# Performance work log

Hardware: AMD Instinct MI355X
Metric: run time of the kernel (lower is better)

The kernel has to match this reference:

```python
import jax, jax.numpy as jnp
import numpy as np

USER_NUM = 100000
ITEM_NUM = 50000
E = 128   # embedding_size
A = 64    # attention_size
M = 8     # memory_size
B = 4096  # batch
NF = 50   # friends per user


def _l2norm(x, axis):
    # torch F.normalize(p=2): x / max(||x||, eps)
    n = jnp.sqrt(jnp.sum(x * x, axis=axis, keepdims=True))
    return x / jnp.maximum(n, 1e-12)


def setup_inputs() -> dict:
    key = jax.random.key(0)
    ks = jax.random.split(key, 9)
    u = lambda k, shape: jax.random.uniform(k, shape, jnp.float32, -0.1, 0.1)
    return {
        "input_u": jax.random.randint(ks[0], (B,), 0, USER_NUM),
        "input_i": jax.random.randint(ks[1], (B,), 0, ITEM_NUM),
        "input_uf": jax.random.randint(ks[2], (B, NF), 0, USER_NUM + 1),
        "uidW": u(ks[3], (USER_NUM + 1, E)),
        "iidW": u(ks[4], (ITEM_NUM, E)),
        "i_bias": jnp.zeros((ITEM_NUM,), jnp.float32),
        "Key": u(ks[5], (E, M)),
        "Mem": jnp.ones((M, E), jnp.float32),
        "WA": u(ks[6], (E, A)),
        "BA": jnp.zeros((A,), jnp.float32),
        "U_omega": u(ks[7], (A, 1)),
    }


def reference(input_u, input_i, input_uf, uidW, iidW, i_bias, Key, Mem, WA, BA, U_omega):
    user_num = uidW.shape[0] - 1  # padding id
    uid = uidW[input_u]                      # [B, E]
    iid = iidW[input_i]                      # [B, E]
    i_b = i_bias[input_i]                    # [B]
    fe = uidW[input_uf]                      # [B, F, E] friend embeddings
    fn = (input_uf != user_num).astype(uid.dtype)  # [B, F] valid-friend mask

    fe = fn[:, :, None] * fe
    uid_n = _l2norm(uid, axis=1)
    fe_n = _l2norm(fe, axis=2)
    cross = uid_n[:, None, :] * fe_n                     # [B, F, E]
    att_key = jnp.einsum('bfe,em->bfm', cross, Key)      # [B, F, M]
    att_mem = jax.nn.softmax(att_key, axis=0)            # softmax over batch (faithful to dim=0)
    att_mem = fn[:, :, None] * att_mem
    f1 = jnp.einsum('bfm,me->bfe', att_mem, Mem)         # [B, F, E]
    f2 = f1 * fe
    h = jax.nn.relu(jnp.einsum('bfe,ea->bfa', f2, WA) + BA)
    j = jnp.exp(jnp.einsum('bfa,ao->bfo', h, U_omega))   # [B, F, 1]
    j = fn[:, :, None] * j
    w = j / (jnp.sum(j, axis=1, keepdims=True) + 1e-8)
    friend = jnp.sum(w * f2, axis=1)                     # [B, E] (dropout p=0 -> identity)
    user = uid + friend
    score = jnp.sum(user * iid, axis=1) + i_b            # [B]
    return score
```

## Files before the change

kernel.cpp:

```cpp
#include <hip/hip_runtime.h>

#define EDIM 128
#define MDIM 8
#define ADIM 64
#define NFR  50
#define NCOL (NFR * MDIM)
#define NPART 256

typedef __attribute__((ext_vector_type(8))) short short8;
typedef __attribute__((ext_vector_type(4))) float f32x4;

__device__ __forceinline__ float waveReduceSum(float v) {
    #pragma unroll
    for (int s = 32; s >= 1; s >>= 1) v += __shfl_xor(v, s, 64);
    return v;
}
__device__ __forceinline__ short f2bf(float x) {
    unsigned u = __float_as_uint(x);
    u += 0x7FFFu + ((u >> 16) & 1u);
    return (short)(u >> 16);
}

__global__ __launch_bounds__(256)
void k0_prep(const float* __restrict__ WA, const float* __restrict__ Mem,
             const float* __restrict__ Key,
             short* __restrict__ WATf, short* __restrict__ MemTf,
             short* __restrict__ KeyTf)
{
    int t = blockIdx.x * 256 + threadIdx.x;
    int lane = t & 63, c = lane & 15, g = (lane >> 4) & 3;
    short8 v = {0, 0, 0, 0, 0, 0, 0, 0};
    if (t < 1024) {
        int frag = t >> 6, Ma = frag >> 2, Kt = frag & 3;
        int a = Ma * 16 + c;
        #pragma unroll
        for (int j = 0; j < 8; ++j) {
            int e = Kt * 32 + g * 8 + j;
            v[j] = f2bf(WA[(size_t)e * ADIM + a]);
        }
        *(short8*)(WATf + (size_t)t * 8) = v;
    } else if (t < 1536) {
        int i = t - 1024, Mt = i >> 6;
        int e = Mt * 16 + c;
        #pragma unroll
        for (int j = 0; j < 8; ++j) {
            int k = g * 8 + j;
            v[j] = (k < MDIM) ? f2bf(Mem[(size_t)k * EDIM + e]) : (short)0;
        }
        *(short8*)(MemTf + (size_t)i * 8) = v;
    } else if (t < 1792) {
        int i = t - 1536, Kt = i >> 6;
        #pragma unroll
        for (int j = 0; j < 8; ++j) {
            int e = Kt * 32 + g * 8 + j;
            v[j] = (c < MDIM) ? f2bf(Key[(size_t)e * MDIM + c]) : (short)0;
        }
        *(short8*)(KeyTf + (size_t)i * 8) = v;
    }
}

__global__ __launch_bounds__(256, 6)
void k1_attkey(const int* __restrict__ input_u, const int* __restrict__ input_uf,
               const float* __restrict__ uidW, const short* __restrict__ KeyTf,
               float* __restrict__ eatt, int user_num)
{
    const int b = blockIdx.x, t = threadIdx.x, w = t >> 6, l = t & 63;
    const int c = l & 15, g = l >> 4;
    __shared__ float uidn[EDIM];
    __shared__ float redW[4];
    __shared__ int ufL[64];

    if (t < 64) ufL[t] = (t < NFR) ? input_uf[(size_t)b * NFR + t] : user_num;
    const int u = input_u[b];
    float x = (t < EDIM) ? uidW[(size_t)u * EDIM + t] : 0.f;
    float ss = waveReduceSum(x * x);
    if (l == 0) redW[w] = ss;
    __syncthreads();
    float uinv = 1.0f / fmaxf(sqrtf(redW[0] + redW[1] + redW[2] + redW[3]), 1e-12f);
    if (t < EDIM) uidn[t] = x * uinv;
    __syncthreads();

    const int f = w * 16 + c;
    const int fid = ufL[f];
    const float fn = (f < NFR && fid != user_num) ? 1.0f : 0.0f;
    const float* fp = uidW + (size_t)fid * EDIM;

    float4 fe[4][2];
    #pragma unroll
    for (int Kt = 0; Kt < 4; ++Kt) {
        fe[Kt][0] = *(const float4*)(fp + Kt * 32 + g * 8);
        fe[Kt][1] = *(const float4*)(fp + Kt * 32 + g * 8 + 4);
    }
    float fss = 0.f;
    #pragma unroll
    for (int Kt = 0; Kt < 4; ++Kt)
        #pragma unroll
        for (int h = 0; h < 2; ++h) {
            float4 q = fe[Kt][h];
            fss += q.x * q.x + q.y * q.y + q.z * q.z + q.w * q.w;
        }
    fss += __shfl_xor(fss, 16, 64);
    fss += __shfl_xor(fss, 32, 64);
    const float inv2 = fn / fmaxf(sqrtf(fss), 1e-12f);

    f32x4 acc = {0.f, 0.f, 0.f, 0.f};
    #pragma unroll
    for (int Kt = 0; Kt < 4; ++Kt) {
        float4 un0 = *(const float4*)&uidn[Kt * 32 + g * 8];
        float4 un1 = *(const float4*)&uidn[Kt * 32 + g * 8 + 4];
        short8 bf;
        bf[0] = f2bf(un0.x * fe[Kt][0].x * inv2);
        bf[1] = f2bf(un0.y * fe[Kt][0].y * inv2);
        bf[2] = f2bf(un0.z * fe[Kt][0].z * inv2);
        bf[3] = f2bf(un0.w * fe[Kt][0].w * inv2);
        bf[4] = f2bf(un1.x * fe[Kt][1].x * inv2);
        bf[5] = f2bf(un1.y * fe[Kt][1].y * inv2);
        bf[6] = f2bf(un1.z * fe[Kt][1].z * inv2);
        bf[7] = f2bf(un1.w * fe[Kt][1].w * inv2);
        short8 af = *(const short8*)(KeyTf + (size_t)(Kt * 64 + l) * 8);
        acc = __builtin_amdgcn_mfma_f32_16x16x32_bf16(af, bf, acc, 0, 0, 0);
    }
    if (f < NFR && g < 2) {
        float4 st = {__expf(acc[0]), __expf(acc[1]), __expf(acc[2]), __expf(acc[3])};
        *(float4*)&eatt[(size_t)b * NCOL + f * MDIM + g * 4] = st;
    }
}

__global__ __launch_bounds__(256)
void k2a_sum(const float* __restrict__ eatt, float* __restrict__ partial, int B)
{
    const int blk = blockIdx.x, t = threadIdx.x, w = t >> 6, l = t & 63;
    __shared__ float colS[4][NCOL];
    const int rowsPerBlk = B / NPART;
    const int rowsPerWave = rowsPerBlk >> 2;
    const int r0 = blk * rowsPerBlk + w * rowsPerWave;

    float4 a1 = {0.f, 0.f, 0.f, 0.f}, a2 = {0.f, 0.f, 0.f, 0.f};
    for (int it = 0; it < rowsPerWave; ++it) {
        const float* row = eatt + (size_t)(r0 + it) * NCOL;
        float4 v1 = *(const float4*)(row + 4 * l);
        a1.x += v1.x; a1.y += v1.y; a1.z += v1.z; a1.w += v1.w;
        if (l < 36) {
            float4 v2 = *(const float4*)(row + 256 + 4 * l);
            a2.x += v2.x; a2.y += v2.y; a2.z += v2.z; a2.w += v2.w;
        }
    }
    *(float4*)&colS[w][4 * l] = a1;
    if (l < 36) *(float4*)&colS[w][256 + 4 * l] = a2;
    __syncthreads();
    if (t < 256)
        partial[(size_t)blk * NCOL + t] =
            colS[0][t] + colS[1][t] + colS[2][t] + colS[3][t];
    if (t < 144) {
        int c2 = 256 + t;
        partial[(size_t)blk * NCOL + c2] =
            colS[0][c2] + colS[1][c2] + colS[2][c2] + colS[3][c2];
    }
}

__global__ __launch_bounds__(512)
void k2b_merge(const float* __restrict__ partial, float* __restrict__ ise)
{
    int c = threadIdx.x;
    if (c >= NCOL) return;
    float S = 0.f;
    for (int b = 0; b < NPART; ++b) S += partial[(size_t)b * NCOL + c];
    ise[c] = 1.0f / S;
}

__global__ __launch_bounds__(256, 6)
void k3_final(const int* __restrict__ input_u, const int* __restrict__ input_i,
              const int* __restrict__ input_uf, const float* __restrict__ uidW,
              const float* __restrict__ iidW, const float* __restrict__ i_bias,
              const short* __restrict__ WATf, const short* __restrict__ MemTf,
              const float* __restrict__ BA, const float* __restrict__ U_omega,
              const float* __restrict__ eatt, const float* __restrict__ ise,
              float* __restrict__ out, int user_num)
{
    const int b = blockIdx.x, t = threadIdx.x, w = t >> 6, l = t & 63;
    const int c = l & 15, g = l >> 4;
    __shared__ short f2s[4][4 * 64 * 8];
    __shared__ float amL[512];
    __shared__ float uidL[EDIM], iidL[EDIM];
    __shared__ float baL[ADIM], uoL[ADIM];
    __shared__ int ufL[64];
    __shared__ float sjW[4], syW[4];

    if (t < 64) ufL[t] = (t < NFR) ? input_uf[(size_t)b * NFR + t] : user_num;
    __syncthreads();

    const int u = input_u[b];
    const int ii = input_i[b];
    if (t < EDIM) {
        uidL[t] = uidW[(size_t)u * EDIM + t];
        iidL[t] = iidW[(size_t)ii * EDIM + t];
    }
    if (t < ADIM) { baL[t] = BA[t]; uoL[t] = U_omega[t]; }

    const int f = w * 16 + c;
    const int fid = ufL[f];
    const float fn = (f < NFR && fid != user_num) ? 1.0f : 0.0f;
    float4 fe4[8];
    {
        const float* fp = uidW + (size_t)fid * EDIM;
        #pragma unroll
        for (int Mt = 0; Mt < 8; ++Mt)
            fe4[Mt] = *(const float4*)(fp + Mt * 16 + g * 4);
    }

    for (int i = t; i < 512; i += 256) {
        float amv = 0.f;
        if (i < NCOL && ufL[i >> 3] != user_num)
            amv = eatt[(size_t)b * NCOL + i] * ise[i];
        amL[i] = amv;
    }
    __syncthreads();

    short8 amf = {0, 0, 0, 0, 0, 0, 0, 0};
    if (g == 0) {
        float4 a0 = *(const float4*)&amL[f * 8];
        float4 a1 = *(const float4*)&amL[f * 8 + 4];
        amf[0] = f2bf(a0.x); amf[1] = f2bf(a0.y);
        amf[2] = f2bf(a0.z); amf[3] = f2bf(a0.w);
        amf[4] = f2bf(a1.x); amf[5] = f2bf(a1.y);
        amf[6] = f2bf(a1.z); amf[7] = f2bf(a1.w);
    }

    f32x4 C1[8];
    #pragma unroll
    for (int Mt = 0; Mt < 8; ++Mt) {
        short8 af = *(const short8*)(MemTf + (size_t)(Mt * 64 + l) * 8);
        f32x4 z = {0.f, 0.f, 0.f, 0.f};
        C1[Mt] = __builtin_amdgcn_mfma_f32_16x16x32_bf16(af, amf, z, 0, 0, 0);
    }

    #pragma unroll
    for (int Mt = 0; Mt < 8; ++Mt) {
        float q0 = C1[Mt][0] * fe4[Mt].x * fn;
        float q1 = C1[Mt][1] * fe4[Mt].y * fn;
        float q2 = C1[Mt][2] * fe4[Mt].z * fn;
        float q3 = C1[Mt][3] * fe4[Mt].w * fn;
        unsigned d0 = ((unsigned)(unsigned short)f2bf(q0)) |
                      (((unsigned)(unsigned short)f2bf(q1)) << 16);
        unsigned d1 = ((unsigned)(unsigned short)f2bf(q2)) |
                      (((unsigned)(unsigned short)f2bf(q3)) << 16);
        int lane2 = ((Mt & 1) * 2 + (g >> 1)) * 16 + c;
        int off = ((Mt >> 1) * 64 + lane2) * 8 + (g & 1) * 4;
        uint2 dd = {d0, d1};
        *(uint2*)&f2s[w][off] = dd;
    }

    f32x4 C2[4], C3 = {0.f, 0.f, 0.f, 0.f};
    #pragma unroll
    for (int Ma = 0; Ma < 4; ++Ma) C2[Ma] = (f32x4){0.f, 0.f, 0.f, 0.f};
    #pragma unroll
    for (int Kt = 0; Kt < 4; ++Kt) {
        short8 bf = *(const short8*)&f2s[w][(Kt * 64 + l) * 8];
        #pragma unroll
        for (int Ma = 0; Ma < 4; ++Ma) {
            short8 af = *(const short8*)(WATf + (size_t)((Ma * 4 + Kt) * 64 + l) * 8);
            C2[Ma] = __builtin_amdgcn_mfma_f32_16x16x32_bf16(af, bf, C2[Ma], 0, 0, 0);
        }
        short8 itf = {0, 0, 0, 0, 0, 0, 0, 0};
        if (c == 0) {
            float4 i0 = *(const float4*)&iidL[Kt * 32 + g * 8];
            float4 i1 = *(const float4*)&iidL[Kt * 32 + g * 8 + 4];
            itf[0] = f2bf(i0.x); itf[1] = f2bf(i0.y);
            itf[2] = f2bf(i0.z); itf[3] = f2bf(i0.w);
            itf[4] = f2bf(i1.x); itf[5] = f2bf(i1.y);
            itf[6] = f2bf(i1.z); itf[7] = f2bf(i1.w);
        }
        C3 = __builtin_amdgcn_mfma_f32_16x16x32_bf16(itf, bf, C3, 0, 0, 0);
    }

    float psum = 0.f;
    #pragma unroll
    for (int Ma = 0; Ma < 4; ++Ma) {
        float4 ba4 = *(const float4*)&baL[Ma * 16 + g * 4];
        float4 uo4 = *(const float4*)&uoL[Ma * 16 + g * 4];
        psum += fmaxf(C2[Ma][0] + ba4.x, 0.f) * uo4.x;
        psum += fmaxf(C2[Ma][1] + ba4.y, 0.f) * uo4.y;
        psum += fmaxf(C2[Ma][2] + ba4.z, 0.f) * uo4.z;
        psum += fmaxf(C2[Ma][3] + ba4.w, 0.f) * uo4.w;
    }
    psum += __shfl_xor(psum, 16, 64);
    psum += __shfl_xor(psum, 32, 64);
    const float jv = (fn > 0.f) ? __expf(psum) : 0.f;
    const float jy = jv * C3[0];
    float sj = waveReduceSum((g == 0) ? jv : 0.f);
    float sy = waveReduceSum(jy);
    if (l == 0) { sjW[w] = sj; syW[w] = sy; }
    __syncthreads();

    if (w == 0) {
        float s = uidL[l] * iidL[l] + uidL[l + 64] * iidL[l + 64];
        s = waveReduceSum(s);
        if (l == 0) {
            float Sj = sjW[0] + sjW[1] + sjW[2] + sjW[3] + 1e-8f;
            float Sy = syW[0] + syW[1] + syW[2] + syW[3];
            out[b] = s + Sy / Sj + i_bias[ii];
        }
    }
}

extern "C" void kernel_launch(void* const* d_in, const int* in_sizes, int n_in,
                              void* d_out, int out_size, void* d_ws, size_t ws_size,
                              hipStream_t stream)
{
    const int*   input_u  = (const int*)d_in[0];
    const int*   input_i  = (const int*)d_in[1];
    const int*   input_uf = (const int*)d_in[2];
    const float* uidW     = (const float*)d_in[3];
    const float* iidW     = (const float*)d_in[4];
    const float* i_bias   = (const float*)d_in[5];
    const float* Key      = (const float*)d_in[6];
    const float* Mem      = (const float*)d_in[7];
    const float* WA       = (const float*)d_in[8];
    const float* BA       = (const float*)d_in[9];
    const float* U_om     = (const float*)d_in[10];

    const int B = in_sizes[0];
    const int user_num = in_sizes[3] / EDIM - 1;

    float* eatt = (float*)d_ws;
    float* partial = eatt + (size_t)B * NCOL;
    float* ise = partial + (size_t)NPART * NCOL;
    short* WATf  = (short*)(ise + NCOL);
    short* MemTf = WATf + 16 * 64 * 8;
    short* KeyTf = MemTf + 8 * 64 * 8;

    k0_prep<<<7, 256, 0, stream>>>(WA, Mem, Key, WATf, MemTf, KeyTf);
    k1_attkey<<<B, 256, 0, stream>>>(input_u, input_uf, uidW, KeyTf, eatt, user_num);
    k2a_sum<<<NPART, 256, 0, stream>>>(eatt, partial, B);
    k2b_merge<<<1, 512, 0, stream>>>(partial, ise);
    k3_final<<<B, 256, 0, stream>>>(input_u, input_i, input_uf, uidW, iidW, i_bias,
                                    WATf, MemTf, BA, U_om, eatt, ise,
                                    (float*)d_out, user_num);
}
```

Baseline: 181.0 us.

## Replace column-sum merge kernel with atomics and cache masked friend embeddings as bf16

Removes the single-block merge kernel. The column sums are now accumulated with atomicAdd into a buffer that the prep kernel zeroes, and the final kernel takes a reciprocal of those sums directly. The attkey kernel also writes the masked friend embeddings as compact bf16 (8192 shorts per batch row). The final kernel reads that buffer instead of re-gathering fp32 rows from the large user table, and it drops the shared-memory staging step for the attention weights. This trades an extra contiguous write and read (about 64 MB of workspace) and nondeterministic atomic ordering for one fewer launch and the removal of random gathers in the final kernel.

```diff
diff --git a/kernel.cpp b/kernel.cpp
--- a/kernel.cpp
+++ b/kernel.cpp
@@ -5,7 +5,7 @@
 #define ADIM 64
 #define NFR  50
 #define NCOL (NFR * MDIM)
-#define NPART 256
+#define NPART 64
 
 typedef __attribute__((ext_vector_type(8))) short short8;
 typedef __attribute__((ext_vector_type(4))) float f32x4;
@@ -20,12 +20,15 @@
     u += 0x7FFFu + ((u >> 16) & 1u);
     return (short)(u >> 16);
 }
+__device__ __forceinline__ float bf2f(short s) {
+    return __uint_as_float(((unsigned)(unsigned short)s) << 16);
+}
 
 __global__ __launch_bounds__(256)
 void k0_prep(const float* __restrict__ WA, const float* __restrict__ Mem,
              const float* __restrict__ Key,
              short* __restrict__ WATf, short* __restrict__ MemTf,
-             short* __restrict__ KeyTf)
+             short* __restrict__ KeyTf, float* __restrict__ S)
 {
     int t = blockIdx.x * 256 + threadIdx.x;
     int lane = t & 63, c = lane & 15, g = (lane >> 4) & 3;
@@ -56,13 +59,15 @@
             v[j] = (c < MDIM) ? f2bf(Key[(size_t)e * MDIM + c]) : (short)0;
         }
         *(short8*)(KeyTf + (size_t)i * 8) = v;
+    } else if (t < 1792 + NCOL) {
+        S[t - 1792] = 0.f;
     }
 }
 
 __global__ __launch_bounds__(256, 6)
 void k1_attkey(const int* __restrict__ input_u, const int* __restrict__ input_uf,
                const float* __restrict__ uidW, const short* __restrict__ KeyTf,
-               float* __restrict__ eatt, int user_num)
+               float* __restrict__ eatt, short* __restrict__ feB, int user_num)
 {
     const int b = blockIdx.x, t = threadIdx.x, w = t >> 6, l = t & 63;
     const int c = l & 15, g = l >> 4;
@@ -103,9 +108,17 @@
     fss += __shfl_xor(fss, 32, 64);
     const float inv2 = fn / fmaxf(sqrtf(fss), 1e-12f);
 
+    short* fbb = feB + (size_t)b * 8192;
     f32x4 acc = {0.f, 0.f, 0.f, 0.f};
     #pragma unroll
     for (int Kt = 0; Kt < 4; ++Kt) {
+        short8 fo;
+        fo[0] = f2bf(fe[Kt][0].x * fn); fo[1] = f2bf(fe[Kt][0].y * fn);
+        fo[2] = f2bf(fe[Kt][0].z * fn); fo[3] = f2bf(fe[Kt][0].w * fn);
+        fo[4] = f2bf(fe[Kt][1].x * fn); fo[5] = f2bf(fe[Kt][1].y * fn);
+        fo[6] = f2bf(fe[Kt][1].z * fn); fo[7] = f2bf(fe[Kt][1].w * fn);
+        *(short8*)(fbb + f * 128 + Kt * 32 + g * 8) = fo;
+
         float4 un0 = *(const float4*)&uidn[Kt * 32 + g * 8];
         float4 un1 = *(const float4*)&uidn[Kt * 32 + g * 8 + 4];
         short8 bf;
@@ -127,7 +140,7 @@
 }
 
 __global__ __launch_bounds__(256)
-void k2a_sum(const float* __restrict__ eatt, float* __restrict__ partial, int B)
+void k2a_sum(const float* __restrict__ eatt, float* __restrict__ S, int B)
 {
     const int blk = blockIdx.x, t = threadIdx.x, w = t >> 6, l = t & 63;
     __shared__ float colS[4][NCOL];
@@ -148,24 +161,8 @@
     *(float4*)&colS[w][4 * l] = a1;
     if (l < 36) *(float4*)&colS[w][256 + 4 * l] = a2;
     __syncthreads();
-    if (t < 256)
-        partial[(size_t)blk * NCOL + t] =
-            colS[0][t] + colS[1][t] + colS[2][t] + colS[3][t];
-    if (t < 144) {
-        int c2 = 256 + t;
-        partial[(size_t)blk * NCOL + c2] =
-            colS[0][c2] + colS[1][c2] + colS[2][c2] + colS[3][c2];
-    }
-}
-
-__global__ __launch_bounds__(512)
-void k2b_merge(const float* __restrict__ partial, float* __restrict__ ise)
-{
-    int c = threadIdx.x;
-    if (c >= NCOL) return;
-    float S = 0.f;
-    for (int b = 0; b < NPART; ++b) S += partial[(size_t)b * NCOL + c];
-    ise[c] = 1.0f / S;
+    for (int i = t; i < NCOL; i += 256)
+        atomicAdd(&S[i], colS[0][i] + colS[1][i] + colS[2][i] + colS[3][i]);
 }
 
 __global__ __launch_bounds__(256, 6)
@@ -174,21 +171,19 @@
               const float* __restrict__ iidW, const float* __restrict__ i_bias,
               const short* __restrict__ WATf, const short* __restrict__ MemTf,
               const float* __restrict__ BA, const float* __restrict__ U_omega,
-              const float* __restrict__ eatt, const float* __restrict__ ise,
-              float* __restrict__ out, int user_num)
+              const float* __restrict__ eatt, const float* __restrict__ S,
+              const short* __restrict__ feB, float* __restrict__ out,
+              int user_num)
 {
     const int b = blockIdx.x, t = threadIdx.x, w = t >> 6, l = t & 63;
     const int c = l & 15, g = l >> 4;
     __shared__ short f2s[4][4 * 64 * 8];
-    __shared__ float amL[512];
     __shared__ float uidL[EDIM], iidL[EDIM];
     __shared__ float baL[ADIM], uoL[ADIM];
     __shared__ int ufL[64];
     __shared__ float sjW[4], syW[4];
 
     if (t < 64) ufL[t] = (t < NFR) ? input_uf[(size_t)b * NFR + t] : user_num;
-    __syncthreads();
-
     const int u = input_u[b];
     const int ii = input_i[b];
     if (t < EDIM) {
@@ -196,34 +191,27 @@
         iidL[t] = iidW[(size_t)ii * EDIM + t];
     }
     if (t < ADIM) { baL[t] = BA[t]; uoL[t] = U_omega[t]; }
+    __syncthreads();
 
     const int f = w * 16 + c;
-    const int fid = ufL[f];
-    const float fn = (f < NFR && fid != user_num) ? 1.0f : 0.0f;
-    float4 fe4[8];
-    {
-        const float* fp = uidW + (size_t)fid * EDIM;
-        #pragma unroll
-        for (int Mt = 0; Mt < 8; ++Mt)
-            fe4[Mt] = *(const float4*)(fp + Mt * 16 + g * 4);
-    }
-
-    for (int i = t; i < 512; i += 256) {
-        float amv = 0.f;
-        if (i < NCOL && ufL[i >> 3] != user_num)
-            amv = eatt[(size_t)b * NCOL + i] * ise[i];
-        amL[i] = amv;
-    }
-    __syncthreads();
+    const float fn = (f < NFR && ufL[f] != user_num) ? 1.0f : 0.0f;
+    const short* fbb = feB + (size_t)b * 8192;
 
     short8 amf = {0, 0, 0, 0, 0, 0, 0, 0};
-    if (g == 0) {
-        float4 a0 = *(const float4*)&amL[f * 8];
-        float4 a1 = *(const float4*)&amL[f * 8 + 4];
-        amf[0] = f2bf(a0.x); amf[1] = f2bf(a0.y);
-        amf[2] = f2bf(a0.z); amf[3] = f2bf(a0.w);
-        amf[4] = f2bf(a1.x); amf[5] = f2bf(a1.y);
-        amf[6] = f2bf(a1.z); amf[7] = f2bf(a1.w);
+    if (g == 0 && fn > 0.f) {
+        const float* ea = eatt + (size_t)b * NCOL + f * 8;
+        float4 e0 = *(const float4*)ea;
+        float4 e1 = *(const float4*)(ea + 4);
+        float4 s0 = *(const float4*)&S[f * 8];
+        float4 s1 = *(const float4*)&S[f * 8 + 4];
+        amf[0] = f2bf(e0.x * __builtin_amdgcn_rcpf(s0.x));
+        amf[1] = f2bf(e0.y * __builtin_amdgcn_rcpf(s0.y));
+        amf[2] = f2bf(e0.z * __builtin_amdgcn_rcpf(s0.z));
+        amf[3] = f2bf(e0.w * __builtin_amdgcn_rcpf(s0.w));
+        amf[4] = f2bf(e1.x * __builtin_amdgcn_rcpf(s1.x));
+        amf[5] = f2bf(e1.y * __builtin_amdgcn_rcpf(s1.y));
+        amf[6] = f2bf(e1.z * __builtin_amdgcn_rcpf(s1.z));
+        amf[7] = f2bf(e1.w * __builtin_amdgcn_rcpf(s1.w));
     }
 
     f32x4 C1[8];
@@ -236,10 +224,11 @@
 
     #pragma unroll
     for (int Mt = 0; Mt < 8; ++Mt) {
-        float q0 = C1[Mt][0] * fe4[Mt].x * fn;
-        float q1 = C1[Mt][1] * fe4[Mt].y * fn;
-        float q2 = C1[Mt][2] * fe4[Mt].z * fn;
-        float q3 = C1[Mt][3] * fe4[Mt].w * fn;
+        uint2 fv = *(const uint2*)(fbb + f * 128 + Mt * 16 + g * 4);
+        float q0 = C1[Mt][0] * bf2f((short)(fv.x & 0xFFFF));
+        float q1 = C1[Mt][1] * bf2f((short)(fv.x >> 16));
+        float q2 = C1[Mt][2] * bf2f((short)(fv.y & 0xFFFF));
+        float q3 = C1[Mt][3] * bf2f((short)(fv.y >> 16));
         unsigned d0 = ((unsigned)(unsigned short)f2bf(q0)) |
                       (((unsigned)(unsigned short)f2bf(q1)) << 16);
         unsigned d1 = ((unsigned)(unsigned short)f2bf(q2)) |
@@ -323,17 +312,16 @@
     const int user_num = in_sizes[3] / EDIM - 1;
 
     float* eatt = (float*)d_ws;
-    float* partial = eatt + (size_t)B * NCOL;
-    float* ise = partial + (size_t)NPART * NCOL;
-    short* WATf  = (short*)(ise + NCOL);
+    float* S    = eatt + (size_t)B * NCOL;
+    short* WATf  = (short*)(S + NCOL);
     short* MemTf = WATf + 16 * 64 * 8;
     short* KeyTf = MemTf + 8 * 64 * 8;
-
-    k0_prep<<<7, 256, 0, stream>>>(WA, Mem, Key, WATf, MemTf, KeyTf);
-    k1_attkey<<<B, 256, 0, stream>>>(input_u, input_uf, uidW, KeyTf, eatt, user_num);
-    k2a_sum<<<NPART, 256, 0, stream>>>(eatt, partial, B);
-    k2b_merge<<<1, 512, 0, stream>>>(partial, ise);
+    short* feB   = KeyTf + 4 * 64 * 8;
+
+    k0_prep<<<9, 256, 0, stream>>>(WA, Mem, Key, WATf, MemTf, KeyTf, S);
+    k1_attkey<<<B, 256, 0, stream>>>(input_u, input_uf, uidW, KeyTf, eatt, feB, user_num);
+    k2a_sum<<<NPART, 256, 0, stream>>>(eatt, S, B);
     k3_final<<<B, 256, 0, stream>>>(input_u, input_i, input_uf, uidW, iidW, i_bias,
-                                    WATf, MemTf, BA, U_om, eatt, ise,
+                                    WATf, MemTf, BA, U_om, eatt, S, feB,
                                     (float*)d_out, user_num);
 }
```

New measurement: 187.9 us. +3.8%, slower.
